# Performance work log

Hardware: AMD Instinct MI355X
Metric: run time of the kernel (lower is better)

## Reference

```python
import jax, jax.numpy as jnp
import numpy as np

N_ITER = 10

def _prelu(x, a):
    return jnp.where(x >= 0, x, a * x)

def _conv2d(x, w, b):
    y = jax.lax.conv_general_dilated(x, w, (1, 1), 'SAME', dimension_numbers=('NCHW', 'OIHW', 'NCHW'))
    return y + b[None, :, None, None]

def _conv3d(x, w, b):
    y = jax.lax.conv_general_dilated(x, w, (1, 1, 1), 'SAME', dimension_numbers=('NCDHW', 'OIDHW', 'NCDHW'))
    return y + b[None, :, None, None, None]

def _forward(dual, primal, g, An, A, dw1, db1, da1, dw2, db2, da2, dw3, db3, pw1, pb1, pa1, pw2, pb2, pa2, pw3, pb3):
    B = primal.shape[0]
    Z, Y, X = primal.shape[2], primal.shape[3], primal.shape[4]
    for k in range(N_ITER):
        # Fortran-order flatten of primal channel 1 -> [B, V] (reshape_fortran((Z*Y*X,1)))
        f_flat = jnp.transpose(primal[:, 1], (0, 3, 2, 1)).reshape(B, -1)
        # batched per-(b, angle) projection matvec: replaces the serialized torch.mm loop
        evalop1 = jnp.einsum('bjdv,bv->bjd', An, f_flat)[:, None]  # [B,1,J,D]
        x = jnp.concatenate([dual, evalop1, g], axis=1)  # 7 channels
        h = _prelu(_conv2d(x, dw1[k], db1[k]), da1[k])
        h = _prelu(_conv2d(h, dw2[k], db2[k]), da2[k])
        dual = dual + _conv2d(h, dw3[k], db3[k])
        # adjoint: sum over angles j of A[b,j] @ dual[b,0,j,:], Fortran-reshaped to (Z,Y,X)
        back = jnp.einsum('bjvd,bjd->bv', A, dual[:, 0])
        evalop2 = jnp.transpose(back.reshape(B, X, Y, Z), (0, 3, 2, 1))[:, None]  # [B,1,Z,Y,X]
        y = jnp.concatenate([primal, evalop2], axis=1)  # 6 channels
        h3 = _prelu(_conv3d(y, pw1[k], pb1[k]), pa1[k])
        h3 = _prelu(_conv3d(h3, pw2[k], pb2[k]), pa2[k])
        primal = primal + _conv3d(h3, pw3[k], pb3[k])
    return primal[:, 0:1]

def setup_inputs():
    key = jax.random.key(0)
    ks = jax.random.split(key, 16)
    B, J, D = 2, 24, 32
    Z = Y = X = 32
    V = Z * Y * X
    NI = N_ITER
    def nrm(k, shape, s=0.05):
        return jax.random.normal(k, shape, jnp.float32) * s
    return {
        'dual': nrm(ks[0], (B, 5, J, D), 1.0),
        'primal': nrm(ks[1], (B, 5, Z, Y, X), 1.0),
        'g': nrm(ks[2], (B, 1, J, D), 1.0),
        'sysm_angles_norm': jax.random.uniform(ks[3], (B, J, D, V), jnp.float32) * 0.01,
        'sysm_angles': jax.random.uniform(ks[4], (B, J, V, D), jnp.float32) * 0.01,
        'dw1': nrm(ks[5], (NI, 32, 7, 3, 3)), 'db1': jnp.zeros((NI, 32), jnp.float32),
        'da1': jnp.full((NI, 1), 0.25, jnp.float32),
        'dw2': nrm(ks[6], (NI, 32, 32, 3, 3)), 'db2': jnp.zeros((NI, 32), jnp.float32),
        'da2': jnp.full((NI, 1), 0.25, jnp.float32),
        'dw3': nrm(ks[7], (NI, 5, 32, 3, 3)), 'db3': jnp.zeros((NI, 5), jnp.float32),
        'pw1': nrm(ks[8], (NI, 32, 6, 3, 3, 3)), 'pb1': jnp.zeros((NI, 32), jnp.float32),
        'pa1': jnp.full((NI, 1), 0.25, jnp.float32),
        'pw2': nrm(ks[9], (NI, 32, 32, 3, 3, 3)), 'pb2': jnp.zeros((NI, 32), jnp.float32),
        'pa2': jnp.full((NI, 1), 0.25, jnp.float32),
        'pw3': nrm(ks[10], (NI, 5, 32, 3, 3, 3)), 'pb3': jnp.zeros((NI, 5), jnp.float32),
        'return_all': 0,
    }

def reference(dual, primal, g, sysm_angles_norm, sysm_angles, dw1, db1, da1, dw2, db2, da2, dw3, db3, pw1, pb1, pa1, pw2, pb2, pa2, pw3, pb3, return_all):
    return _forward(dual, primal, g, sysm_angles_norm, sysm_angles, dw1, db1, da1, dw2, db2, da2, dw3, db3, pw1, pb1, pa1, pw2, pb2, pa2, pw3, pb3)
```

## Files before the change

kernel.cpp:

```cpp
#include <hip/hip_runtime.h>
#include <cstdint>
#include <cstddef>

#define DEV __device__ __forceinline__

constexpr int B_  = 2;
constexpr int J_  = 24;
constexpr int D_  = 32;
constexpr int V_  = 32768;
constexpr int JD_ = J_ * D_;
constexpr int NI_ = 10;
constexpr long long ANN = 50331648LL;

typedef __attribute__((ext_vector_type(8))) short bf16x8;
typedef __attribute__((ext_vector_type(4))) float f32x4;

DEV float bflo(unsigned q){ return __uint_as_float(q << 16); }
DEV float bfhi(unsigned q){ return __uint_as_float(q & 0xffff0000u); }
DEV unsigned short f2bf(float f){
  unsigned u = __float_as_uint(f);
  unsigned r = (u + 0x7fffu + ((u >> 16) & 1u)) >> 16;
  return (unsigned short)r;
}
DEV float bf2f(unsigned short h){ return __uint_as_float((unsigned)h << 16); }
DEV void split2(float v, unsigned short& h, unsigned short& l){
  h = f2bf(v);
  l = f2bf(v - bf2f(h));
}

__global__ __launch_bounds__(256) void k_convert(const float* __restrict__ src,
                                                 unsigned short* __restrict__ dst, int n8){
  int t = blockIdx.x * 256 + threadIdx.x;
  if (t >= n8) return;
  const float4* s4 = (const float4*)src;
  float4 a = s4[2*t], b = s4[2*t+1];
  uint4 o;
  o.x = (unsigned)f2bf(a.x) | ((unsigned)f2bf(a.y) << 16);
  o.y = (unsigned)f2bf(a.z) | ((unsigned)f2bf(a.w) << 16);
  o.z = (unsigned)f2bf(b.x) | ((unsigned)f2bf(b.y) << 16);
  o.w = (unsigned)f2bf(b.z) | ((unsigned)f2bf(b.w) << 16);
  ((uint4*)dst)[t] = o;
}

__global__ __launch_bounds__(256) void k_permute_f(const float* __restrict__ primal,
                                                   float* __restrict__ f){
  const int t = blockIdx.x * 256 + threadIdx.x;
  const int b = t >> 15, v = t & 32767;
  const int x = v >> 10, y = (v >> 5) & 31, z = v & 31;
  f[t] = primal[((b*5 + 1) << 15) + (z << 10) + (y << 5) + x];
}

__global__ __launch_bounds__(256) void k_evalop1_bf(const unsigned short* __restrict__ AnB,
                                                    const float* __restrict__ f_flat,
                                                    float* __restrict__ ev1){
  const int jd = blockIdx.x, b = blockIdx.y;
  const int row = b * JD_ + jd;
  const uint4*  ap = (const uint4*)(AnB + (size_t)row * V_);
  const float4* fp = (const float4*)(f_flat + b * V_);
  float acc = 0.0f;
  for (int i = threadIdx.x; i < V_/8; i += 256){
    uint4 q = ap[i];
    float4 fa = fp[2*i], fb = fp[2*i+1];
    acc += bflo(q.x)*fa.x + bfhi(q.x)*fa.y + bflo(q.y)*fa.z + bfhi(q.y)*fa.w;
    acc += bflo(q.z)*fb.x + bfhi(q.z)*fb.y + bflo(q.w)*fb.z + bfhi(q.w)*fb.w;
  }
  #pragma unroll
  for (int off = 32; off > 0; off >>= 1) acc += __shfl_down(acc, off);
  __shared__ float red[4];
  if ((threadIdx.x & 63) == 0) red[threadIdx.x >> 6] = acc;
  __syncthreads();
  if (threadIdx.x == 0) ev1[row] = red[0] + red[1] + red[2] + red[3];
}

__global__ __launch_bounds__(256) void k_evalop1_f32(const float* __restrict__ An,
                                                     const float* __restrict__ f_flat,
                                                     float* __restrict__ ev1){
  const int jd = blockIdx.x, b = blockIdx.y;
  const int row = b * JD_ + jd;
  const float4* ap = (const float4*)(An + (size_t)row * V_);
  const float4* fp = (const float4*)(f_flat + b * V_);
  float acc = 0.0f;
  for (int i = threadIdx.x; i < V_/4; i += 256){
    float4 av = ap[i], fv = fp[i];
    acc += av.x*fv.x + av.y*fv.y + av.z*fv.z + av.w*fv.w;
  }
  #pragma unroll
  for (int off = 32; off > 0; off >>= 1) acc += __shfl_down(acc, off);
  __shared__ float red[4];
  if ((threadIdx.x & 63) == 0) red[threadIdx.x >> 6] = acc;
  __syncthreads();
  if (threadIdx.x == 0) ev1[row] = red[0] + red[1] + red[2] + red[3];
}

template<int CIN, int COUT, bool PRELU, bool ADDTO>
__global__ __launch_bounds__(256) void k_conv2d(const float* __restrict__ in,
                                                const float* __restrict__ ev1,
                                                const float* __restrict__ g,
                                                const float* __restrict__ w,
                                                const float* __restrict__ bias,
                                                const float* __restrict__ alpha,
                                                float* __restrict__ out){
  const int t = blockIdx.x * 256 + threadIdx.x;
  const int d = t & 31;
  const int j = (t >> 5) % J_;
  const int rest = (t >> 5) / J_;
  const int o = rest % COUT;
  const int b = rest / COUT;
  float acc = bias[o];
  for (int ci = 0; ci < CIN; ci++){
    const float* ip;
    if constexpr (CIN == 7){
      ip = (ci < 5) ? (in + (b*5 + ci)*JD_) : ((ci == 5) ? (ev1 + b*JD_) : (g + b*JD_));
    } else {
      ip = in + (b*CIN + ci)*JD_;
    }
    const float* wp = w + (o*CIN + ci)*9;
    #pragma unroll
    for (int kh = 0; kh < 3; kh++){
      const int jj = j + kh - 1;
      if ((unsigned)jj < (unsigned)J_){
        #pragma unroll
        for (int kw = 0; kw < 3; kw++){
          const int dd = d + kw - 1;
          if ((unsigned)dd < 32u)
            acc += ip[jj*32 + dd] * wp[kh*3 + kw];
        }
      }
    }
  }
  if constexpr (PRELU){
    const float a = alpha[0];
    acc = (acc >= 0.0f) ? acc : a * acc;
  }
  if constexpr (ADDTO) out[t] += acc;
  else                 out[t] = acc;
}

__global__ __launch_bounds__(256) void k_back_bf(const unsigned short* __restrict__ AB,
                                                 const float* __restrict__ dual,
                                                 float* __restrict__ ev2){
  __shared__ float wj[JD_];
  const int b = blockIdx.y;
  for (int i = threadIdx.x; i < JD_; i += 256) wj[i] = dual[b*5*JD_ + i];
  __syncthreads();
  const int lane = threadIdx.x & 63;
  const int wave = threadIdx.x >> 6;
  const int dq = lane & 7;
  const int vi = lane >> 3;
  const int v = blockIdx.x * 32 + wave * 8 + vi;
  float acc = 0.0f;
  for (int j = 0; j < J_; j++){
    const unsigned short* rp = AB + ((size_t)(b*J_ + j) * V_ + v) * 32 + dq*4;
    uint2 q = *(const uint2*)rp;
    const float* wp = &wj[j*32 + dq*4];
    acc += bflo(q.x)*wp[0] + bfhi(q.x)*wp[1] + bflo(q.y)*wp[2] + bfhi(q.y)*wp[3];
  }
  acc += __shfl_xor(acc, 1);
  acc += __shfl_xor(acc, 2);
  acc += __shfl_xor(acc, 4);
  if (dq == 0){
    const int xx = v >> 10, yy = (v >> 5) & 31, zz = v & 31;
    ev2[(b << 15) + (zz << 10) + (yy << 5) + xx] = acc;
  }
}

__global__ __launch_bounds__(256) void k_back_f32(const float* __restrict__ A,
                                                  const float* __restrict__ dual,
                                                  float* __restrict__ ev2){
  __shared__ float wj[JD_];
  const int b = blockIdx.y;
  for (int i = threadIdx.x; i < JD_; i += 256) wj[i] = dual[b*5*JD_ + i];
  __syncthreads();
  const int lane = threadIdx.x & 63;
  const int wave = threadIdx.x >> 6;
  const int dq = lane & 7;
  const int vi = lane >> 3;
  const int v = blockIdx.x * 32 + wave * 8 + vi;
  float acc = 0.0f;
  for (int j = 0; j < J_; j++){
    const float* rp = A + ((size_t)(b*J_ + j) * V_ + v) * 32 + dq*4;
    float4 av = *(const float4*)rp;
    const float* wp = &wj[j*32 + dq*4];
    acc += av.x*wp[0] + av.y*wp[1] + av.z*wp[2] + av.w*wp[3];
  }
  acc += __shfl_xor(acc, 1);
  acc += __shfl_xor(acc, 2);
  acc += __shfl_xor(acc, 4);
  if (dq == 0){
    const int xx = v >> 10, yy = (v >> 5) & 31, zz = v & 31;
    ev2[(b << 15) + (zz << 10) + (yy << 5) + xx] = acc;
  }
}


__global__ __launch_bounds__(256) void k_wprep_l1(const float* __restrict__ pw,
    unsigned short* __restrict__ wfH, unsigned short* __restrict__ wfL){
  const int t = blockIdx.x * 256 + threadIdx.x;
  if (t >= NI_*9*2*64) return;
  const int k = t / 1152, rem = t % 1152;
  const int tap9 = rem >> 7, r2 = rem & 127;
  const int nt = r2 >> 6, lane = r2 & 63;
  const int co = nt*16 + (lane & 15);
  const int kx = lane >> 4;
  const size_t ob = (size_t)((k*9 + tap9)*2 + nt)*512 + lane*8;
  #pragma unroll
  for (int e = 0; e < 8; e++){
    const int ci = e;
    float v = 0.0f;
    if (kx < 3 && ci < 6)
      v = pw[(size_t)k*5184 + (size_t)(co*6 + ci)*27 + tap9*3 + kx];
    unsigned short h, l; split2(v, h, l);
    wfH[ob + e] = h; wfL[ob + e] = l;
  }
}

__global__ __launch_bounds__(256) void k_wprep_l2(const float* __restrict__ pw,
    unsigned short* __restrict__ wfH, unsigned short* __restrict__ wfL){
  const int t = blockIdx.x * 256 + threadIdx.x;
  if (t >= NI_*27*2*64) return;
  const int k = t / 3456, rem = t % 3456;
  const int tap = rem >> 7, r2 = rem & 127;
  const int nt = r2 >> 6, lane = r2 & 63;
  const int co = nt*16 + (lane & 15);
  const int cib = (lane >> 4) * 8;
  const size_t ob = (size_t)((k*27 + tap)*2 + nt)*512 + lane*8;
  #pragma unroll
  for (int e = 0; e < 8; e++){
    const float v = pw[(size_t)k*27648 + (size_t)(co*32 + cib + e)*27 + tap];
    unsigned short h, l; split2(v, h, l);
    wfH[ob + e] = h; wfL[ob + e] = l;
  }
}

__global__ __launch_bounds__(256) void k_wprep_l3(const float* __restrict__ pw,
    unsigned short* __restrict__ wfH, unsigned short* __restrict__ wfL){
  const int t = blockIdx.x * 256 + threadIdx.x;
  if (t >= NI_*27*64) return;
  const int k = t / 1728, rem = t % 1728;
  const int tap = rem >> 6, lane = rem & 63;
  const int co = lane & 15;
  const int cib = (lane >> 4) * 8;
  const size_t ob = (size_t)(k*27 + tap)*512 + lane*8;
  #pragma unroll
  for (int e = 0; e < 8; e++){
    float v = 0.0f;
    if (co < 5)
      v = pw[(size_t)k*4320 + (size_t)(co*32 + cib + e)*27 + tap];
    unsigned short h, l; split2(v, h, l);
    wfH[ob + e] = h; wfL[ob + e] = l;
  }
}

__global__ __launch_bounds__(256) void k_prep_l1(const float* __restrict__ primal,
                                                 const float* __restrict__ ev2,
                                                 unsigned short* __restrict__ outH,
                                                 unsigned short* __restrict__ outL){
  const int t = blockIdx.x * 256 + threadIdx.x;
  const int b = t >> 15, s = t & 32767;
  const int z = s >> 10, y = (s >> 5) & 31, x = s & 31;
  unsigned H[4], L[4];
  #pragma unroll
  for (int p = 0; p < 4; p++){
    const int c0 = p*2, c1 = p*2 + 1;
    float v0 = (c0 < 5) ? primal[((b*5 + c0) << 15) + s] : ((c0 == 5) ? ev2[(b << 15) + s] : 0.0f);
    float v1 = (c1 < 5) ? primal[((b*5 + c1) << 15) + s] : ((c1 == 5) ? ev2[(b << 15) + s] : 0.0f);
    unsigned short h0, l0, h1, l1;
    split2(v0, h0, l0); split2(v1, h1, l1);
    H[p] = (unsigned)h0 | ((unsigned)h1 << 16);
    L[p] = (unsigned)l0 | ((unsigned)l1 << 16);
  }
  const size_t idx = (size_t)((b*34 + z + 1)*34 + (y + 1))*288 + (size_t)(x + 1)*8;
  *(uint4*)(outH + idx) = make_uint4(H[0], H[1], H[2], H[3]);
  *(uint4*)(outL + idx) = make_uint4(L[0], L[1], L[2], L[3]);
}

__global__ __launch_bounds__(256, 2) void k_c3l1(
    const unsigned short* __restrict__ inH, const unsigned short* __restrict__ inL,
    const unsigned short* __restrict__ wfH, const unsigned short* __restrict__ wfL,
    const float* __restrict__ bias, const float* __restrict__ alpha,
    unsigned short* __restrict__ outH, unsigned short* __restrict__ outL)
{
  const int lane = threadIdx.x & 63;
  const int w = blockIdx.x * 4 + (threadIdx.x >> 6);
  const int y = w & 31, z = (w >> 5) & 31, b = w >> 10;
  const int lm = lane & 15, lg = lane >> 4;
  const float bv0 = bias[lm], bv1 = bias[16 + lm];
  f32x4 acc[2][2];
  #pragma unroll
  for (int x2 = 0; x2 < 2; x2++){
    acc[x2][0] = {bv0, bv0, bv0, bv0};
    acc[x2][1] = {bv1, bv1, bv1, bv1};
  }
  for (int kz = 0; kz < 3; kz++){
    #pragma unroll
    for (int ky = 0; ky < 3; ky++){
      const int tap = kz*3 + ky;
      const size_t rb = (size_t)((b*34 + z + kz)*34 + (y + ky)) * 288;
      const bf16x8 bh0 = *(const bf16x8*)(wfH + (size_t)(tap*2 + 0)*512 + lane*8);
      const bf16x8 bh1 = *(const bf16x8*)(wfH + (size_t)(tap*2 + 1)*512 + lane*8);
      const bf16x8 bl0 = *(const bf16x8*)(wfL + (size_t)(tap*2 + 0)*512 + lane*8);
      const bf16x8 bl1 = *(const bf16x8*)(wfL + (size_t)(tap*2 + 1)*512 + lane*8);
      #pragma unroll
      for (int x2 = 0; x2 < 2; x2++){
        const size_t off = rb + (size_t)(x2*16 + lm + lg) * 8;
        const bf16x8 ah = *(const bf16x8*)(inH + off);
        const bf16x8 al = *(const bf16x8*)(inL + off);
        acc[x2][0] = __builtin_amdgcn_mfma_f32_16x16x32_bf16(ah, bh0, acc[x2][0], 0, 0, 0);
        acc[x2][1] = __builtin_amdgcn_mfma_f32_16x16x32_bf16(ah, bh1, acc[x2][1], 0, 0, 0);
        acc[x2][0] = __builtin_amdgcn_mfma_f32_16x16x32_bf16(al, bh0, acc[x2][0], 0, 0, 0);
        acc[x2][1] = __builtin_amdgcn_mfma_f32_16x16x32_bf16(al, bh1, acc[x2][1], 0, 0, 0);
        acc[x2][0] = __builtin_amdgcn_mfma_f32_16x16x32_bf16(ah, bl0, acc[x2][0], 0, 0, 0);
        acc[x2][1] = __builtin_amdgcn_mfma_f32_16x16x32_bf16(ah, bl1, acc[x2][1], 0, 0, 0);
      }
    }
  }
  const float a0 = alpha[0];
  const size_t ob = (size_t)((b*34 + z + 1)*34 + (y + 1)) * 1088;
  #pragma unroll
  for (int x2 = 0; x2 < 2; x2++){
    #pragma unroll
    for (int nt = 0; nt < 2; nt++){
      const int co = nt*16 + lm;
      #pragma unroll
      for (int r = 0; r < 4; r++){
        float v = acc[x2][nt][r];
        v = (v >= 0.0f) ? v : a0 * v;
        unsigned short h, l; split2(v, h, l);
        const size_t idx = ob + (size_t)(x2*16 + lg*4 + r + 1)*32 + co;
        outH[idx] = h; outL[idx] = l;
      }
    }
  }
}

__global__ __launch_bounds__(256, 2) void k_c3l2(
    const unsigned short* __restrict__ inH, const unsigned short* __restrict__ inL,
    const unsigned short* __restrict__ wfH, const unsigned short* __restrict__ wfL,
    const float* __restrict__ bias, const float* __restrict__ alpha,
    unsigned short* __restrict__ outH, unsigned short* __restrict__ outL)
{
  const int lane = threadIdx.x & 63;
  const int w = blockIdx.x * 4 + (threadIdx.x >> 6);
  const int y = w & 31, z = (w >> 5) & 31, b = w >> 10;
  const int lm = lane & 15, lg = lane >> 4;
  const float bv0 = bias[lm], bv1 = bias[16 + lm];
  f32x4 acc[2][2];
  #pragma unroll
  for (int x2 = 0; x2 < 2; x2++){
    acc[x2][0] = {bv0, bv0, bv0, bv0};
    acc[x2][1] = {bv1, bv1, bv1, bv1};
  }
  for (int kz = 0; kz < 3; kz++){
    for (int ky = 0; ky < 3; ky++){
      const size_t rb = (size_t)((b*34 + z + kz)*34 + (y + ky)) * 1088;
      #pragma unroll
      for (int kx = 0; kx < 3; kx++){
        const int tap = (kz*3 + ky)*3 + kx;
        const bf16x8 bh0 = *(const bf16x8*)(wfH + (size_t)(tap*2 + 0)*512 + lane*8);
        const bf16x8 bh1 = *(const bf16x8*)(wfH + (size_t)(tap*2 + 1)*512 + lane*8);
        const bf16x8 bl0 = *(const bf16x8*)(wfL + (size_t)(tap*2 + 0)*512 + lane*8);
        const bf16x8 bl1 = *(const bf16x8*)(wfL + (size_t)(tap*2 + 1)*512 + lane*8);
        #pragma unroll
        for (int x2 = 0; x2 < 2; x2++){
          const size_t off = rb + (size_t)(x2*16 + lm + kx)*32 + lg*8;
          const bf16x8 ah = *(const bf16x8*)(inH + off);
          const bf16x8 al = *(const bf16x8*)(inL + off);
          acc[x2][0] = __builtin_amdgcn_mfma_f32_16x16x32_bf16(ah, bh0, acc[x2][0], 0, 0, 0);
          acc[x2][1] = __builtin_amdgcn_mfma_f32_16x16x32_bf16(ah, bh1, acc[x2][1], 0, 0, 0);
          acc[x2][0] = __builtin_amdgcn_mfma_f32_16x16x32_bf16(al, bh0, acc[x2][0], 0, 0, 0);
          acc[x2][1] = __builtin_amdgcn_mfma_f32_16x16x32_bf16(al, bh1, acc[x2][1], 0, 0, 0);
          acc[x2][0] = __builtin_amdgcn_mfma_f32_16x16x32_bf16(ah, bl0, acc[x2][0], 0, 0, 0);
          acc[x2][1] = __builtin_amdgcn_mfma_f32_16x16x32_bf16(ah, bl1, acc[x2][1], 0, 0, 0);
        }
      }
    }
  }
  const float a0 = alpha[0];
  const size_t ob = (size_t)((b*34 + z + 1)*34 + (y + 1)) * 1088;
  #pragma unroll
  for (int x2 = 0; x2 < 2; x2++){
    #pragma unroll
    for (int nt = 0; nt < 2; nt++){
      const int co = nt*16 + lm;
      #pragma unroll
      for (int r = 0; r < 4; r++){
        float v = acc[x2][nt][r];
        v = (v >= 0.0f) ? v : a0 * v;
        unsigned short h, l; split2(v, h, l);
        const size_t idx = ob + (size_t)(x2*16 + lg*4 + r + 1)*32 + co;
        outH[idx] = h; outL[idx] = l;
      }
    }
  }
}

__global__ __launch_bounds__(256, 2) void k_c3l3(
    const unsigned short* __restrict__ inH, const unsigned short* __restrict__ inL,
    const unsigned short* __restrict__ wfH, const unsigned short* __restrict__ wfL,
    const float* __restrict__ bias,
    float* __restrict__ primal)
{
  const int lane = threadIdx.x & 63;
  const int w = blockIdx.x * 4 + (threadIdx.x >> 6);
  const int y = w & 31, z = (w >> 5) & 31, b = w >> 10;
  const int lm = lane & 15, lg = lane >> 4;
  const float bv = (lm < 5) ? bias[lm] : 0.0f;
  f32x4 acc[2];
  acc[0] = {bv, bv, bv, bv};
  acc[1] = {bv, bv, bv, bv};
  for (int kz = 0; kz < 3; kz++){
    for (int ky = 0; ky < 3; ky++){
      const size_t rb = (size_t)((b*34 + z + kz)*34 + (y + ky)) * 1088;
      #pragma unroll
      for (int kx = 0; kx < 3; kx++){
        const int tap = (kz*3 + ky)*3 + kx;
        const bf16x8 bh = *(const bf16x8*)(wfH + (size_t)tap*512 + lane*8);
        const bf16x8 bl = *(const bf16x8*)(wfL + (size_t)tap*512 + lane*8);
        #pragma unroll
        for (int x2 = 0; x2 < 2; x2++){
          const size_t off = rb + (size_t)(x2*16 + lm + kx)*32 + lg*8;
          const bf16x8 ah = *(const bf16x8*)(inH + off);
          const bf16x8 al = *(const bf16x8*)(inL + off);
          acc[x2] = __builtin_amdgcn_mfma_f32_16x16x32_bf16(ah, bh, acc[x2], 0, 0, 0);
          acc[x2] = __builtin_amdgcn_mfma_f32_16x16x32_bf16(al, bh, acc[x2], 0, 0, 0);
          acc[x2] = __builtin_amdgcn_mfma_f32_16x16x32_bf16(ah, bl, acc[x2], 0, 0, 0);
        }
      }
    }
  }
  if (lm < 5){
    float* pp = primal + ((size_t)(b*5 + lm) << 15) + (z << 10) + (y << 5);
    #pragma unroll
    for (int x2 = 0; x2 < 2; x2++){
      #pragma unroll
      for (int r = 0; r < 4; r++){
        const int x = x2*16 + lg*4 + r;
        pp[x] += acc[x2][r];
      }
    }
  }
}

__global__ __launch_bounds__(256) void k_output(const float* __restrict__ primal,
                                                float* __restrict__ out){
  const int t = blockIdx.x * 256 + threadIdx.x;
  const int b = t >> 15, s = t & 32767;
  out[t] = primal[((b*5) << 15) + s];
}

extern "C" void kernel_launch(void* const* d_in, const int* in_sizes, int n_in,
                              void* d_out, int out_size, void* d_ws, size_t ws_size,
                              hipStream_t stream){
  const float* dual_in   = (const float*)d_in[0];
  const float* primal_in = (const float*)d_in[1];
  const float* g    = (const float*)d_in[2];
  const float* An   = (const float*)d_in[3];
  const float* A    = (const float*)d_in[4];
  const float* dw1  = (const float*)d_in[5];
  const float* db1  = (const float*)d_in[6];
  const float* da1  = (const float*)d_in[7];
  const float* dw2  = (const float*)d_in[8];
  const float* db2  = (const float*)d_in[9];
  const float* da2  = (const float*)d_in[10];
  const float* dw3  = (const float*)d_in[11];
  const float* db3  = (const float*)d_in[12];
  const float* pw1  = (const float*)d_in[13];
  const float* pb1  = (const float*)d_in[14];
  const float* pa1  = (const float*)d_in[15];
  const float* pw2  = (const float*)d_in[16];
  const float* pb2  = (const float*)d_in[17];
  const float* pa2  = (const float*)d_in[18];
  const float* pw3  = (const float*)d_in[19];
  const float* pb3  = (const float*)d_in[20];

  constexpr size_t L1_SZ  = 2ull*34*34*36*8;
  constexpr size_t H3_SZ  = 2ull*34*34*34*32;
  constexpr size_t WF1_SZ = (size_t)NI_*9*2*512;
  constexpr size_t WF2_SZ = (size_t)NI_*27*2*512;
  constexpr size_t WF3_SZ = (size_t)NI_*27*512;
  constexpr size_t CONV_USH = 2*L1_SZ + 4*H3_SZ + 2*WF1_SZ + 2*WF2_SZ + 2*WF3_SZ;
  constexpr size_t F_FLOATS = 7680 + 327680 + 65536 + 1536 + 49152 + 49152 + 65536;

  const size_t bf_bytes = (size_t)ANN * 2u * 2u;
  const bool use_bf16 = ws_size >= bf_bytes + CONV_USH*2 + F_FLOATS*4;

  unsigned short* AnB = (unsigned short*)d_ws;
  unsigned short* AB  = AnB + ANN;
  unsigned short* u0 = use_bf16 ? (AB + ANN) : (unsigned short*)d_ws;
  unsigned short* L1H  = u0;
  unsigned short* L1L  = L1H + L1_SZ;
  unsigned short* H3AH = L1L + L1_SZ;
  unsigned short* H3AL = H3AH + H3_SZ;
  unsigned short* H3BH = H3AL + H3_SZ;
  unsigned short* H3BL = H3BH + H3_SZ;
  unsigned short* WF1H = H3BL + H3_SZ;
  unsigned short* WF1L = WF1H + WF1_SZ;
  unsigned short* WF2H = WF1L + WF1_SZ;
  unsigned short* WF2L = WF2H + WF2_SZ;
  unsigned short* WF3H = WF2L + WF2_SZ;
  unsigned short* WF3L = WF3H + WF3_SZ;

  float* base = (float*)(WF3L + WF3_SZ);
  float* dual   = base;
  float* primal = dual + 7680;
  float* f_flat = primal + 327680;
  float* ev1    = f_flat + 65536;
  float* h2a    = ev1 + 1536;
  float* h2b    = h2a + 49152;
  float* ev2    = h2b + 49152;

  hipMemcpyAsync(dual, dual_in, 7680 * sizeof(float), hipMemcpyDeviceToDevice, stream);
  hipMemcpyAsync(primal, primal_in, 327680 * sizeof(float), hipMemcpyDeviceToDevice, stream);

  if (use_bf16){
    const int n8 = (int)(ANN / 8);
    k_convert<<<n8 / 256, 256, 0, stream>>>(An, AnB, n8);
    k_convert<<<n8 / 256, 256, 0, stream>>>(A,  AB,  n8);
  }

  hipMemsetAsync(L1H, 0, (2*L1_SZ + 4*H3_SZ) * sizeof(unsigned short), stream);

  k_wprep_l1<<<(NI_*9*2*64  + 255)/256, 256, 0, stream>>>(pw1, WF1H, WF1L);
  k_wprep_l2<<<(NI_*27*2*64 + 255)/256, 256, 0, stream>>>(pw2, WF2H, WF2L);
  k_wprep_l3<<<(NI_*27*64   + 255)/256, 256, 0, stream>>>(pw3, WF3H, WF3L);

  for (int k = 0; k < NI_; k++){
    k_permute_f<<<256, 256, 0, stream>>>(primal, f_flat);
    if (use_bf16) k_evalop1_bf <<<dim3(JD_, B_), 256, 0, stream>>>(AnB, f_flat, ev1);
    else          k_evalop1_f32<<<dim3(JD_, B_), 256, 0, stream>>>(An,  f_flat, ev1);

    k_conv2d<7, 32, true,  false><<<192, 256, 0, stream>>>(dual, ev1, g,
        dw1 + k*2016, db1 + k*32, da1 + k, h2a);
    k_conv2d<32, 32, true, false><<<192, 256, 0, stream>>>(h2a, nullptr, nullptr,
        dw2 + k*9216, db2 + k*32, da2 + k, h2b);
    k_conv2d<32, 5, false, true><<<30, 256, 0, stream>>>(h2b, nullptr, nullptr,
        dw3 + k*1440, db3 + k*5, nullptr, dual);

    if (use_bf16) k_back_bf <<<dim3(V_/32, B_), 256, 0, stream>>>(AB, dual, ev2);
    else          k_back_f32<<<dim3(V_/32, B_), 256, 0, stream>>>(A,  dual, ev2);

    k_prep_l1<<<256, 256, 0, stream>>>(primal, ev2, L1H, L1L);
    k_c3l1<<<512, 256, 0, stream>>>(L1H, L1L, WF1H + (size_t)k*9*2*512, WF1L + (size_t)k*9*2*512,
                                    pb1 + k*32, pa1 + k, H3AH, H3AL);
    k_c3l2<<<512, 256, 0, stream>>>(H3AH, H3AL, WF2H + (size_t)k*27*2*512, WF2L + (size_t)k*27*2*512,
                                    pb2 + k*32, pa2 + k, H3BH, H3BL);
    k_c3l3<<<512, 256, 0, stream>>>(H3BH, H3BL, WF3H + (size_t)k*27*512, WF3L + (size_t)k*27*512,
                                    pb3 + k*5, primal);
  }

  k_output<<<256, 256, 0, stream>>>(primal, (float*)d_out);
}
```

Baseline: 2.202 ms.

## Fuse dual-branch conv stack, merge backprojection with layer prep, fold permute into conv3

Result: slower. 4.440 ms (+101.6%).

```diff
diff --git a/kernel.cpp b/kernel.cpp
--- a/kernel.cpp
+++ b/kernel.cpp
@@ -28,10 +28,15 @@
   l = f2bf(v - bf2f(h));
 }
 
-__global__ __launch_bounds__(256) void k_convert(const float* __restrict__ src,
-                                                 unsigned short* __restrict__ dst, int n8){
+__global__ __launch_bounds__(256) void k_convert2(const float* __restrict__ srcA,
+                                                  const float* __restrict__ srcB,
+                                                  unsigned short* __restrict__ dstA,
+                                                  unsigned short* __restrict__ dstB,
+                                                  int n8){
   int t = blockIdx.x * 256 + threadIdx.x;
-  if (t >= n8) return;
+  const float* src; unsigned short* dst;
+  if (t < n8){ src = srcA; dst = dstA; }
+  else       { src = srcB; dst = dstB; t -= n8; }
   const float4* s4 = (const float4*)src;
   float4 a = s4[2*t], b = s4[2*t+1];
   uint4 o;
@@ -92,53 +97,113 @@
   if (threadIdx.x == 0) ev1[row] = red[0] + red[1] + red[2] + red[3];
 }
 
-template<int CIN, int COUT, bool PRELU, bool ADDTO>
-__global__ __launch_bounds__(256) void k_conv2d(const float* __restrict__ in,
-                                                const float* __restrict__ ev1,
-                                                const float* __restrict__ g,
-                                                const float* __restrict__ w,
-                                                const float* __restrict__ bias,
-                                                const float* __restrict__ alpha,
-                                                float* __restrict__ out){
-  const int t = blockIdx.x * 256 + threadIdx.x;
-  const int d = t & 31;
-  const int j = (t >> 5) % J_;
-  const int rest = (t >> 5) / J_;
-  const int o = rest % COUT;
-  const int b = rest / COUT;
-  float acc = bias[o];
-  for (int ci = 0; ci < CIN; ci++){
-    const float* ip;
-    if constexpr (CIN == 7){
-      ip = (ci < 5) ? (in + (b*5 + ci)*JD_) : ((ci == 5) ? (ev1 + b*JD_) : (g + b*JD_));
-    } else {
-      ip = in + (b*CIN + ci)*JD_;
-    }
-    const float* wp = w + (o*CIN + ci)*9;
-    #pragma unroll
-    for (int kh = 0; kh < 3; kh++){
-      const int jj = j + kh - 1;
-      if ((unsigned)jj < (unsigned)J_){
+__global__ __launch_bounds__(256) void k_dualconv(
+    const float* __restrict__ dcur,
+    const float* __restrict__ ev1,
+    const float* __restrict__ g,
+    const float* __restrict__ w1, const float* __restrict__ b1, const float* __restrict__ a1,
+    const float* __restrict__ w2, const float* __restrict__ b2, const float* __restrict__ a2,
+    const float* __restrict__ w3, const float* __restrict__ b3,
+    float* __restrict__ dnxt)
+{
+  __shared__ float x7[7][7][32];
+  __shared__ float h1[32][5][32];
+  __shared__ float h2[32][3][32];
+  const int b  = blockIdx.x / J_;
+  const int j0 = blockIdx.x % J_;
+  const int t  = threadIdx.x;
+
+  for (int idx = t; idx < 7*7*32; idx += 256){
+    const int d = idx & 31, jr = (idx >> 5) % 7, ci = idx / (7*32);
+    const int j = j0 - 3 + jr;
+    float v = 0.0f;
+    if ((unsigned)j < (unsigned)J_){
+      if (ci < 5)       v = dcur[((b*5 + ci)*J_ + j)*32 + d];
+      else if (ci == 5) v = ev1[(b*J_ + j)*32 + d];
+      else              v = g[(b*J_ + j)*32 + d];
+    }
+    x7[ci][jr][d] = v;
+  }
+  __syncthreads();
+
+  {
+    const float al = a1[0];
+    for (int idx = t; idx < 32*5*32; idx += 256){
+      const int d = idx & 31, r1 = (idx >> 5) % 5, co = idx / (5*32);
+      const int j = j0 - 2 + r1;
+      float acc = 0.0f;
+      if ((unsigned)j < (unsigned)J_){
+        acc = b1[co];
+        for (int ci = 0; ci < 7; ci++){
+          const float* wp = w1 + (co*7 + ci)*9;
+          #pragma unroll
+          for (int kh = 0; kh < 3; kh++){
+            const int jr = r1 + kh;
+            #pragma unroll
+            for (int kw = 0; kw < 3; kw++){
+              const int dd = d + kw - 1;
+              if ((unsigned)dd < 32u) acc += x7[ci][jr][dd] * wp[kh*3 + kw];
+            }
+          }
+        }
+        acc = (acc >= 0.0f) ? acc : al * acc;
+      }
+      h1[co][r1][d] = acc;
+    }
+  }
+  __syncthreads();
+
+  {
+    const float al = a2[0];
+    for (int idx = t; idx < 32*3*32; idx += 256){
+      const int d = idx & 31, r2 = (idx >> 5) % 3, co = idx / (3*32);
+      const int j = j0 - 1 + r2;
+      float acc = 0.0f;
+      if ((unsigned)j < (unsigned)J_){
+        acc = b2[co];
+        for (int ci = 0; ci < 32; ci++){
+          const float* wp = w2 + (co*32 + ci)*9;
+          #pragma unroll
+          for (int kh = 0; kh < 3; kh++){
+            const int r1 = r2 + kh;
+            #pragma unroll
+            for (int kw = 0; kw < 3; kw++){
+              const int dd = d + kw - 1;
+              if ((unsigned)dd < 32u) acc += h1[ci][r1][dd] * wp[kh*3 + kw];
+            }
+          }
+        }
+        acc = (acc >= 0.0f) ? acc : al * acc;
+      }
+      h2[co][r2][d] = acc;
+    }
+  }
+  __syncthreads();
+
+  for (int idx = t; idx < 5*32; idx += 256){
+    const int d = idx & 31, co = idx >> 5;
+    float acc = b3[co];
+    for (int ci = 0; ci < 32; ci++){
+      const float* wp = w3 + (co*32 + ci)*9;
+      #pragma unroll
+      for (int kh = 0; kh < 3; kh++){
         #pragma unroll
         for (int kw = 0; kw < 3; kw++){
           const int dd = d + kw - 1;
-          if ((unsigned)dd < 32u)
-            acc += ip[jj*32 + dd] * wp[kh*3 + kw];
+          if ((unsigned)dd < 32u) acc += h2[ci][kh][dd] * wp[kh*3 + kw];
         }
       }
     }
-  }
-  if constexpr (PRELU){
-    const float a = alpha[0];
-    acc = (acc >= 0.0f) ? acc : a * acc;
-  }
-  if constexpr (ADDTO) out[t] += acc;
-  else                 out[t] = acc;
-}
-
-__global__ __launch_bounds__(256) void k_back_bf(const unsigned short* __restrict__ AB,
-                                                 const float* __restrict__ dual,
-                                                 float* __restrict__ ev2){
+    const int o = ((b*5 + co)*J_ + j0)*32 + d;
+    dnxt[o] = dcur[o] + acc;
+  }
+}
+
+__global__ __launch_bounds__(256) void k_backprep_bf(const unsigned short* __restrict__ AB,
+                                                     const float* __restrict__ dual,
+                                                     const float* __restrict__ primal,
+                                                     unsigned short* __restrict__ L1H,
+                                                     unsigned short* __restrict__ L1L){
   __shared__ float wj[JD_];
   const int b = blockIdx.y;
   for (int i = threadIdx.x; i < JD_; i += 256) wj[i] = dual[b*5*JD_ + i];
@@ -160,13 +225,31 @@
   acc += __shfl_xor(acc, 4);
   if (dq == 0){
     const int xx = v >> 10, yy = (v >> 5) & 31, zz = v & 31;
-    ev2[(b << 15) + (zz << 10) + (yy << 5) + xx] = acc;
-  }
-}
-
-__global__ __launch_bounds__(256) void k_back_f32(const float* __restrict__ A,
-                                                  const float* __restrict__ dual,
-                                                  float* __restrict__ ev2){
+    const int s = (zz << 10) + (yy << 5) + xx;
+    float vals[8];
+    #pragma unroll
+    for (int c = 0; c < 5; c++) vals[c] = primal[((b*5 + c) << 15) + s];
+    vals[5] = acc; vals[6] = 0.0f; vals[7] = 0.0f;
+    unsigned H[4], L[4];
+    #pragma unroll
+    for (int p = 0; p < 4; p++){
+      unsigned short h0, l0, h1_, l1_;
+      split2(vals[2*p],   h0, l0);
+      split2(vals[2*p+1], h1_, l1_);
+      H[p] = (unsigned)h0 | ((unsigned)h1_ << 16);
+      L[p] = (unsigned)l0 | ((unsigned)l1_ << 16);
+    }
+    const size_t idx = (size_t)((b*34 + zz + 1)*34 + (yy + 1))*288 + (size_t)(xx + 1)*8;
+    *(uint4*)(L1H + idx) = make_uint4(H[0], H[1], H[2], H[3]);
+    *(uint4*)(L1L + idx) = make_uint4(L[0], L[1], L[2], L[3]);
+  }
+}
+
+__global__ __launch_bounds__(256) void k_backprep_f32(const float* __restrict__ A,
+                                                      const float* __restrict__ dual,
+                                                      const float* __restrict__ primal,
+                                                      unsigned short* __restrict__ L1H,
+                                                      unsigned short* __restrict__ L1L){
   __shared__ float wj[JD_];
   const int b = blockIdx.y;
   for (int i = threadIdx.x; i < JD_; i += 256) wj[i] = dual[b*5*JD_ + i];
@@ -188,7 +271,23 @@
   acc += __shfl_xor(acc, 4);
   if (dq == 0){
     const int xx = v >> 10, yy = (v >> 5) & 31, zz = v & 31;
-    ev2[(b << 15) + (zz << 10) + (yy << 5) + xx] = acc;
+    const int s = (zz << 10) + (yy << 5) + xx;
+    float vals[8];
+    #pragma unroll
+    for (int c = 0; c < 5; c++) vals[c] = primal[((b*5 + c) << 15) + s];
+    vals[5] = acc; vals[6] = 0.0f; vals[7] = 0.0f;
+    unsigned H[4], L[4];
+    #pragma unroll
+    for (int p = 0; p < 4; p++){
+      unsigned short h0, l0, h1_, l1_;
+      split2(vals[2*p],   h0, l0);
+      split2(vals[2*p+1], h1_, l1_);
+      H[p] = (unsigned)h0 | ((unsigned)h1_ << 16);
+      L[p] = (unsigned)l0 | ((unsigned)l1_ << 16);
+    }
+    const size_t idx = (size_t)((b*34 + zz + 1)*34 + (yy + 1))*288 + (size_t)(xx + 1)*8;
+    *(uint4*)(L1H + idx) = make_uint4(H[0], H[1], H[2], H[3]);
+    *(uint4*)(L1L + idx) = make_uint4(L[0], L[1], L[2], L[3]);
   }
 }
 
@@ -251,28 +350,7 @@
   }
 }
 
-__global__ __launch_bounds__(256) void k_prep_l1(const float* __restrict__ primal,
-                                                 const float* __restrict__ ev2,
-                                                 unsigned short* __restrict__ outH,
-                                                 unsigned short* __restrict__ outL){
-  const int t = blockIdx.x * 256 + threadIdx.x;
-  const int b = t >> 15, s = t & 32767;
-  const int z = s >> 10, y = (s >> 5) & 31, x = s & 31;
-  unsigned H[4], L[4];
-  #pragma unroll
-  for (int p = 0; p < 4; p++){
-    const int c0 = p*2, c1 = p*2 + 1;
-    float v0 = (c0 < 5) ? primal[((b*5 + c0) << 15) + s] : ((c0 == 5) ? ev2[(b << 15) + s] : 0.0f);
-    float v1 = (c1 < 5) ? primal[((b*5 + c1) << 15) + s] : ((c1 == 5) ? ev2[(b << 15) + s] : 0.0f);
-    unsigned short h0, l0, h1, l1;
-    split2(v0, h0, l0); split2(v1, h1, l1);
-    H[p] = (unsigned)h0 | ((unsigned)h1 << 16);
-    L[p] = (unsigned)l0 | ((unsigned)l1 << 16);
-  }
-  const size_t idx = (size_t)((b*34 + z + 1)*34 + (y + 1))*288 + (size_t)(x + 1)*8;
-  *(uint4*)(outH + idx) = make_uint4(H[0], H[1], H[2], H[3]);
-  *(uint4*)(outL + idx) = make_uint4(L[0], L[1], L[2], L[3]);
-}
+DEV int xcd_swz512(int bid){ return ((bid & 7) << 6) | (bid >> 3); }
 
 __global__ __launch_bounds__(256, 2) void k_c3l1(
     const unsigned short* __restrict__ inH, const unsigned short* __restrict__ inL,
@@ -281,7 +359,7 @@
     unsigned short* __restrict__ outH, unsigned short* __restrict__ outL)
 {
   const int lane = threadIdx.x & 63;
-  const int w = blockIdx.x * 4 + (threadIdx.x >> 6);
+  const int w = xcd_swz512(blockIdx.x) * 4 + (threadIdx.x >> 6);
   const int y = w & 31, z = (w >> 5) & 31, b = w >> 10;
   const int lm = lane & 15, lg = lane >> 4;
   const float bv0 = bias[lm], bv1 = bias[16 + lm];
@@ -340,7 +418,7 @@
     unsigned short* __restrict__ outH, unsigned short* __restrict__ outL)
 {
   const int lane = threadIdx.x & 63;
-  const int w = blockIdx.x * 4 + (threadIdx.x >> 6);
+  const int w = xcd_swz512(blockIdx.x) * 4 + (threadIdx.x >> 6);
   const int y = w & 31, z = (w >> 5) & 31, b = w >> 10;
   const int lm = lane & 15, lg = lane >> 4;
   const float bv0 = bias[lm], bv1 = bias[16 + lm];
@@ -398,10 +476,11 @@
     const unsigned short* __restrict__ inH, const unsigned short* __restrict__ inL,
     const unsigned short* __restrict__ wfH, const unsigned short* __restrict__ wfL,
     const float* __restrict__ bias,
-    float* __restrict__ primal)
+    float* __restrict__ primal,
+    float* __restrict__ f_flat)
 {
   const int lane = threadIdx.x & 63;
-  const int w = blockIdx.x * 4 + (threadIdx.x >> 6);
+  const int w = xcd_swz512(blockIdx.x) * 4 + (threadIdx.x >> 6);
   const int y = w & 31, z = (w >> 5) & 31, b = w >> 10;
   const int lm = lane & 15, lg = lane >> 4;
   const float bv = (lm < 5) ? bias[lm] : 0.0f;
@@ -435,7 +514,10 @@
       #pragma unroll
       for (int r = 0; r < 4; r++){
         const int x = x2*16 + lg*4 + r;
-        pp[x] += acc[x2][r];
+        const float nv = pp[x] + acc[x2][r];
+        pp[x] = nv;
+        if (lm == 1)
+          f_flat[(b << 15) + (x << 10) + (y << 5) + z] = nv;
       }
     }
   }
@@ -479,7 +561,7 @@
   constexpr size_t WF2_SZ = (size_t)NI_*27*2*512;
   constexpr size_t WF3_SZ = (size_t)NI_*27*512;
   constexpr size_t CONV_USH = 2*L1_SZ + 4*H3_SZ + 2*WF1_SZ + 2*WF2_SZ + 2*WF3_SZ;
-  constexpr size_t F_FLOATS = 7680 + 327680 + 65536 + 1536 + 49152 + 49152 + 65536;
+  constexpr size_t F_FLOATS = 2*7680 + 327680 + 65536 + 1536;
 
   const size_t bf_bytes = (size_t)ANN * 2u * 2u;
   const bool use_bf16 = ws_size >= bf_bytes + CONV_USH*2 + F_FLOATS*4;
@@ -501,21 +583,18 @@
   unsigned short* WF3L = WF3H + WF3_SZ;
 
   float* base = (float*)(WF3L + WF3_SZ);
-  float* dual   = base;
-  float* primal = dual + 7680;
+  float* dual_a = base;
+  float* dual_b = dual_a + 7680;
+  float* primal = dual_b + 7680;
   float* f_flat = primal + 327680;
   float* ev1    = f_flat + 65536;
-  float* h2a    = ev1 + 1536;
-  float* h2b    = h2a + 49152;
-  float* ev2    = h2b + 49152;
-
-  hipMemcpyAsync(dual, dual_in, 7680 * sizeof(float), hipMemcpyDeviceToDevice, stream);
+
+  hipMemcpyAsync(dual_a, dual_in, 7680 * sizeof(float), hipMemcpyDeviceToDevice, stream);
   hipMemcpyAsync(primal, primal_in, 327680 * sizeof(float), hipMemcpyDeviceToDevice, stream);
 
   if (use_bf16){
     const int n8 = (int)(ANN / 8);
-    k_convert<<<n8 / 256, 256, 0, stream>>>(An, AnB, n8);
-    k_convert<<<n8 / 256, 256, 0, stream>>>(A,  AB,  n8);
+    k_convert2<<<2*n8 / 256, 256, 0, stream>>>(An, A, AnB, AB, n8);
   }
 
   hipMemsetAsync(L1H, 0, (2*L1_SZ + 4*H3_SZ) * sizeof(unsigned short), stream);
@@ -524,28 +603,30 @@
   k_wprep_l2<<<(NI_*27*2*64 + 255)/256, 256, 0, stream>>>(pw2, WF2H, WF2L);
   k_wprep_l3<<<(NI_*27*64   + 255)/256, 256, 0, stream>>>(pw3, WF3H, WF3L);
 
+  k_permute_f<<<256, 256, 0, stream>>>(primal, f_flat);
+
+  float* dcur = dual_a;
+  float* dnxt = dual_b;
   for (int k = 0; k < NI_; k++){
-    k_permute_f<<<256, 256, 0, stream>>>(primal, f_flat);
     if (use_bf16) k_evalop1_bf <<<dim3(JD_, B_), 256, 0, stream>>>(AnB, f_flat, ev1);
     else          k_evalop1_f32<<<dim3(JD_, B_), 256, 0, stream>>>(An,  f_flat, ev1);
 
-    k_conv2d<7, 32, true,  false><<<192, 256, 0, stream>>>(dual, ev1, g,
-        dw1 + k*2016, db1 + k*32, da1 + k, h2a);
-    k_conv2d<32, 32, true, false><<<192, 256, 0, stream>>>(h2a, nullptr, nullptr,
-        dw2 + k*9216, db2 + k*32, da2 + k, h2b);
-    k_conv2d<32, 5, false, true><<<30, 256, 0, stream>>>(h2b, nullptr, nullptr,
-        dw3 + k*1440, db3 + k*5, nullptr, dual);
-
-    if (use_bf16) k_back_bf <<<dim3(V_/32, B_), 256, 0, stream>>>(AB, dual, ev2);
-    else          k_back_f32<<<dim3(V_/32, B_), 256, 0, stream>>>(A,  dual, ev2);
-
-    k_prep_l1<<<256, 256, 0, stream>>>(primal, ev2, L1H, L1L);
+    k_dualconv<<<B_*J_, 256, 0, stream>>>(dcur, ev1, g,
+        dw1 + k*2016, db1 + k*32, da1 + k,
+        dw2 + k*9216, db2 + k*32, da2 + k,
+        dw3 + k*1440, db3 + k*5, dnxt);
+
+    if (use_bf16) k_backprep_bf <<<dim3(V_/32, B_), 256, 0, stream>>>(AB, dnxt, primal, L1H, L1L);
+    else          k_backprep_f32<<<dim3(V_/32, B_), 256, 0, stream>>>(A,  dnxt, primal, L1H, L1L);
+
     k_c3l1<<<512, 256, 0, stream>>>(L1H, L1L, WF1H + (size_t)k*9*2*512, WF1L + (size_t)k*9*2*512,
                                     pb1 + k*32, pa1 + k, H3AH, H3AL);
     k_c3l2<<<512, 256, 0, stream>>>(H3AH, H3AL, WF2H + (size_t)k*27*2*512, WF2L + (size_t)k*27*2*512,
                                     pb2 + k*32, pa2 + k, H3BH, H3BL);
     k_c3l3<<<512, 256, 0, stream>>>(H3BH, H3BL, WF3H + (size_t)k*27*512, WF3L + (size_t)k*27*512,
-                                    pb3 + k*5, primal);
+                                    pb3 + k*5, primal, f_flat);
+
+    float* tmp = dcur; dcur = dnxt; dnxt = tmp;
   }
 
   k_output<<<256, 256, 0, stream>>>(primal, (float*)d_out);
```
